# Kernel tuning notes

Measured on AMD Instinct MI355X. Metric: run time of the kernel, lower is better.

Reference implementation:

```python
import jax, jax.numpy as jnp
import numpy as np

BS, D, H = 65536, 768, 12
DK = D // H // 2  # 32
EPS = 1e-6

def setup_inputs() -> dict:
    key = jax.random.key(0)
    ks = jax.random.split(key, 4)
    scale = 1.0 / np.sqrt(D)
    return {
        "x": jax.random.normal(ks[0], (BS, D), dtype=jnp.float32),
        "Wq": jax.random.normal(ks[1], (D, D), dtype=jnp.float32) * scale,
        "Wk": jax.random.normal(ks[2], (D, D), dtype=jnp.float32) * scale,
        "Wv": jax.random.normal(ks[3], (D, D), dtype=jnp.float32) * scale,
        "gamma": jnp.ones((D,), dtype=jnp.float32),
        "beta": jnp.zeros((D,), dtype=jnp.float32),
    }

def reference(x, Wq, Wk, Wv, gamma, beta):
    bs = x.shape[0]
    # LayerNorm (eps=1e-6)
    mu = jnp.mean(x, axis=-1, keepdims=True)
    var = jnp.mean(jnp.square(x - mu), axis=-1, keepdims=True)
    xn = (x - mu) / jnp.sqrt(var + EPS) * gamma + beta
    # QKV projections (nn.Linear, no bias: y = x @ W.T), split feature dim as (h, 2, d_k)
    q = (xn @ Wq.T).reshape(bs, H, 2, DK)
    k = (xn @ Wk.T).reshape(bs, H, 2, DK)
    v = (xn @ Wv.T).reshape(bs, H, 2, DK)
    # tiny 2x2 attention per head
    scores = jnp.einsum('bhpd,bhqd->bhpq', q, k) / np.sqrt(DK)
    attn = jax.nn.softmax(scores, axis=-1)
    out = jnp.einsum('bhpq,bhqd->bhpd', attn, v).reshape(bs, D)
    return out + x
```

## Files before the change

kernel.cpp:

```cpp
#include <hip/hip_runtime.h>

typedef _Float16 f16;
typedef _Float16 f16x8 __attribute__((ext_vector_type(8)));
typedef _Float16 f16x4 __attribute__((ext_vector_type(4)));
typedef float f32x16 __attribute__((ext_vector_type(16)));

#define BS 65536
#define D 768
#define H 12
#define RB 256
#define NBLK ((BS / RB) * H)
#define W_ELEMS ((size_t)D * D)
#define XN_ELEMS ((size_t)BS * D)

typedef const __attribute__((address_space(1))) void gvoid_t;
typedef __attribute__((address_space(3))) void lvoid_t;

__global__ __launch_bounds__(256, 4) void ln_kernel(const float* __restrict__ x,
                                                    const float* __restrict__ gamma,
                                                    const float* __restrict__ beta,
                                                    f16* __restrict__ xn) {
  int wave = threadIdx.x >> 6, lane = threadIdx.x & 63;
  size_t row = (size_t)blockIdx.x * 4 + wave;
  const float4* xr = (const float4*)(x + row * D) + lane * 3;
  float4 v0 = xr[0], v1 = xr[1], v2 = xr[2];
  float sum = (v0.x + v0.y) + (v0.z + v0.w) + (v1.x + v1.y) + (v1.z + v1.w)
            + (v2.x + v2.y) + (v2.z + v2.w);
  float sq = v0.x*v0.x + v0.y*v0.y + v0.z*v0.z + v0.w*v0.w
           + v1.x*v1.x + v1.y*v1.y + v1.z*v1.z + v1.w*v1.w
           + v2.x*v2.x + v2.y*v2.y + v2.z*v2.z + v2.w*v2.w;
#pragma unroll
  for (int d2 = 1; d2 <= 32; d2 <<= 1) {
    sum += __shfl_xor(sum, d2, 64);
    sq  += __shfl_xor(sq,  d2, 64);
  }
  float mu   = sum * (1.0f / D);
  float rstd = rsqrtf(sq * (1.0f / D) - mu * mu + 1e-6f);
  const float4* g4 = (const float4*)(gamma) + lane * 3;
  const float4* b4 = (const float4*)(beta)  + lane * 3;
  float4 g0 = g4[0], g1 = g4[1], g2 = g4[2];
  float4 b0 = b4[0], b1 = b4[1], b2 = b4[2];
  f16* xo = xn + row * D + lane * 12;
  f16x4 o0, o1, o2;
  o0[0] = (f16)((v0.x - mu) * rstd * g0.x + b0.x);
  o0[1] = (f16)((v0.y - mu) * rstd * g0.y + b0.y);
  o0[2] = (f16)((v0.z - mu) * rstd * g0.z + b0.z);
  o0[3] = (f16)((v0.w - mu) * rstd * g0.w + b0.w);
  o1[0] = (f16)((v1.x - mu) * rstd * g1.x + b1.x);
  o1[1] = (f16)((v1.y - mu) * rstd * g1.y + b1.y);
  o1[2] = (f16)((v1.z - mu) * rstd * g1.z + b1.z);
  o1[3] = (f16)((v1.w - mu) * rstd * g1.w + b1.w);
  o2[0] = (f16)((v2.x - mu) * rstd * g2.x + b2.x);
  o2[1] = (f16)((v2.y - mu) * rstd * g2.y + b2.y);
  o2[2] = (f16)((v2.z - mu) * rstd * g2.z + b2.z);
  o2[3] = (f16)((v2.w - mu) * rstd * g2.w + b2.w);
  *(f16x4*)(xo)     = o0;
  *(f16x4*)(xo + 4) = o1;
  *(f16x4*)(xo + 8) = o2;
}

__global__ __launch_bounds__(256, 4) void wconv_kernel(const float* __restrict__ Wq,
                                                       const float* __restrict__ Wk,
                                                       const float* __restrict__ Wv,
                                                       f16* __restrict__ wf) {
  int b = blockIdx.x;
  int m = b / 288;
  size_t e = ((size_t)(b % 288) * 256 + threadIdx.x) * 8;
  const float* src = (m == 0 ? Wq : (m == 1 ? Wk : Wv)) + e;
  float4 v0 = *(const float4*)src;
  float4 v1 = *(const float4*)(src + 4);
  f16x8 o;
  o[0] = (f16)v0.x; o[1] = (f16)v0.y; o[2] = (f16)v0.z; o[3] = (f16)v0.w;
  o[4] = (f16)v1.x; o[5] = (f16)v1.y; o[6] = (f16)v1.z; o[7] = (f16)v1.w;
  *(f16x8*)(wf + (size_t)m * W_ELEMS + e) = o;
}

__global__ __launch_bounds__(256, 2) void qkv_attn_kernel(const f16* __restrict__ xn,
                                                          const f16* __restrict__ wf,
                                                          const float* __restrict__ x,
                                                          float* __restrict__ out) {
  __shared__ f16 sB[2][192 * 64] __attribute__((aligned(16)));

  const int tid  = threadIdx.x;
  const int wave = tid >> 6;
  const int lane = tid & 63;
  const int l31  = lane & 31;
  const int hi   = lane >> 5;

  int bid = blockIdx.x;
  int my  = (bid & 7) * (NBLK / 8) + (bid >> 3);
  int rb  = my / H;
  int h   = my % H;

  unsigned offs[6];
  {
    int rl = wave * 48 + (lane & 7);
    int c  = lane >> 3;
#pragma unroll
    for (int o = 0; o < 6; ++o) {
      int r = rl + o * 8;
      offs[o] = (unsigned)((r >> 6) * (int)W_ELEMS + (h * 64 + (r & 63)) * D + c * 8);
    }
  }

  const int rbase = (l31 >> 3) * 512 + hi * 64 + (l31 & 7) * 8;

  const f16* ap0 = xn + ((size_t)rb * RB + wave * 64 + l31) * D + hi * 8;
  const f16* ap1 = ap0 + (size_t)32 * D;

#define STAGE(KO, BUF)                                                                   \
  {                                                                                      \
    const f16* bp = wf + (KO) * 64;                                                      \
    _Pragma("unroll") for (int o = 0; o < 6; ++o) {                                      \
      __builtin_amdgcn_global_load_lds((gvoid_t*)(bp + offs[o]),                         \
                                       (lvoid_t*)(&sB[BUF][(wave * 6 + o) * 512]),       \
                                       16, 0, 0);                                        \
    }                                                                                    \
  }

  STAGE(0, 0);

  f32x16 acc[6][2];
#pragma unroll
  for (int t = 0; t < 6; ++t)
#pragma unroll
    for (int rt = 0; rt < 2; ++rt)
#pragma unroll
      for (int i = 0; i < 16; ++i) acc[t][rt][i] = 0.f;

  __syncthreads();

#pragma unroll
  for (int ko = 0; ko < 12; ++ko) {
    const int cur = ko & 1;
    if (ko < 11) STAGE(ko + 1, cur ^ 1);
    __builtin_amdgcn_sched_barrier(0);

    const f16* bb = &sB[cur][rbase];
    __builtin_amdgcn_s_setprio(1);
#pragma unroll
    for (int s = 0; s < 4; ++s) {
      f16x8 a0 = *(const f16x8*)(ap0 + ko * 64 + s * 16);
      f16x8 a1 = *(const f16x8*)(ap1 + ko * 64 + s * 16);
#pragma unroll
      for (int t = 0; t < 6; ++t) {
        f16x8 b = *(const f16x8*)(bb + t * 2048 + s * 128);
        acc[t][0] = __builtin_amdgcn_mfma_f32_32x32x16_f16(a0, b, acc[t][0], 0, 0, 0);
        acc[t][1] = __builtin_amdgcn_mfma_f32_32x32x16_f16(a1, b, acc[t][1], 0, 0, 0);
      }
    }
    __builtin_amdgcn_s_setprio(0);
    if (ko < 11) __syncthreads();
  }

  {
    const float scale = 0.17677669529663687f;
#pragma unroll
    for (int rt = 0; rt < 2; ++rt) {
      const size_t grow0 = (size_t)rb * RB + wave * 64 + rt * 32;
#pragma unroll
      for (int g = 0; g < 16; ++g) {
        float q0 = acc[0][rt][g], q1 = acc[1][rt][g];
        float k0 = acc[2][rt][g], k1 = acc[3][rt][g];
        float s00 = q0 * k0, s01 = q0 * k1, s10 = q1 * k0, s11 = q1 * k1;
#pragma unroll
        for (int d2 = 1; d2 <= 16; d2 <<= 1) {
          s00 += __shfl_xor(s00, d2, 64);
          s01 += __shfl_xor(s01, d2, 64);
          s10 += __shfl_xor(s10, d2, 64);
          s11 += __shfl_xor(s11, d2, 64);
        }
        s00 *= scale; s01 *= scale; s10 *= scale; s11 *= scale;
        float mx0 = fmaxf(s00, s01);
        float e00 = __expf(s00 - mx0), e01 = __expf(s01 - mx0);
        float r0 = 1.0f / (e00 + e01);
        float a00 = e00 * r0, a01 = e01 * r0;
        float mx1 = fmaxf(s10, s11);
        float e10 = __expf(s10 - mx1), e11 = __expf(s11 - mx1);
        float r1 = 1.0f / (e10 + e11);
        float a10 = e10 * r1, a11 = e11 * r1;

        int row_w = (g & 3) + 8 * (g >> 2) + 4 * hi;
        const float* xp = x   + (grow0 + row_w) * D + h * 64 + l31;
        float*       op = out + (grow0 + row_w) * D + h * 64 + l31;
        float v0 = acc[4][rt][g], v1 = acc[5][rt][g];
        op[0]  = a00 * v0 + a01 * v1 + xp[0];
        op[32] = a10 * v0 + a11 * v1 + xp[32];
      }
    }
  }
#undef STAGE
}

extern "C" void kernel_launch(void* const* d_in, const int* in_sizes, int n_in,
                              void* d_out, int out_size, void* d_ws, size_t ws_size,
                              hipStream_t stream) {
  const float* x     = (const float*)d_in[0];
  const float* Wq    = (const float*)d_in[1];
  const float* Wk    = (const float*)d_in[2];
  const float* Wv    = (const float*)d_in[3];
  const float* gamma = (const float*)d_in[4];
  const float* beta  = (const float*)d_in[5];
  float* out = (float*)d_out;
  (void)in_sizes; (void)n_in; (void)out_size; (void)ws_size;

  f16* xn = (f16*)d_ws;
  f16* wf = xn + XN_ELEMS;

  ln_kernel<<<dim3(BS / 4), dim3(256), 0, stream>>>(x, gamma, beta, xn);
  wconv_kernel<<<dim3(864), dim3(256), 0, stream>>>(Wq, Wk, Wv, wf);
  qkv_attn_kernel<<<dim3(NBLK), dim3(256), 0, stream>>>(xn, wf, x, out);
}
```

Baseline: 712.6 us.

## Stage A tiles through swizzled LDS, halve row block, coalesce LN stores

The QKV kernel now loads the activation tile into LDS with global_load_lds, double-buffered like the weights. Both A and B tiles get an XOR swizzle, and the row block per workgroup drops from 256 to 128, so each wave does one 32-row MFMA tile. The __syncthreads calls are replaced with explicit vmcnt waits and s_barrier. LayerNorm now handles two rows per wave and stages the fp16 output through LDS for 16-byte coalesced stores. Halving the row block doubles how often the weight slice is refetched per row, and the hand-written waitcnt counts must match the number of issued loads.

Result: no change. 723.4 us (+1.5%).

```diff
diff --git a/kernel.cpp b/kernel.cpp
--- a/kernel.cpp
+++ b/kernel.cpp
@@ -8,7 +8,7 @@
 #define BS 65536
 #define D 768
 #define H 12
-#define RB 256
+#define RB 128
 #define NBLK ((BS / RB) * H)
 #define W_ELEMS ((size_t)D * D)
 #define XN_ELEMS ((size_t)BS * D)
@@ -20,43 +20,62 @@
                                                     const float* __restrict__ gamma,
                                                     const float* __restrict__ beta,
                                                     f16* __restrict__ xn) {
+  __shared__ f16 sRow[4][2 * D];
   int wave = threadIdx.x >> 6, lane = threadIdx.x & 63;
-  size_t row = (size_t)blockIdx.x * 4 + wave;
-  const float4* xr = (const float4*)(x + row * D) + lane * 3;
-  float4 v0 = xr[0], v1 = xr[1], v2 = xr[2];
-  float sum = (v0.x + v0.y) + (v0.z + v0.w) + (v1.x + v1.y) + (v1.z + v1.w)
-            + (v2.x + v2.y) + (v2.z + v2.w);
-  float sq = v0.x*v0.x + v0.y*v0.y + v0.z*v0.z + v0.w*v0.w
-           + v1.x*v1.x + v1.y*v1.y + v1.z*v1.z + v1.w*v1.w
-           + v2.x*v2.x + v2.y*v2.y + v2.z*v2.z + v2.w*v2.w;
+  size_t row0 = ((size_t)blockIdx.x * 4 + wave) * 2;
+  const float4* xr0 = (const float4*)(x + row0 * D) + lane * 3;
+  const float4* xr1 = (const float4*)(x + (row0 + 1) * D) + lane * 3;
+  float4 u0 = xr0[0], u1 = xr0[1], u2 = xr0[2];
+  float4 w0 = xr1[0], w1 = xr1[1], w2 = xr1[2];
+
+  float s0 = (u0.x + u0.y) + (u0.z + u0.w) + (u1.x + u1.y) + (u1.z + u1.w)
+           + (u2.x + u2.y) + (u2.z + u2.w);
+  float q0 = u0.x*u0.x + u0.y*u0.y + u0.z*u0.z + u0.w*u0.w
+           + u1.x*u1.x + u1.y*u1.y + u1.z*u1.z + u1.w*u1.w
+           + u2.x*u2.x + u2.y*u2.y + u2.z*u2.z + u2.w*u2.w;
+  float s1 = (w0.x + w0.y) + (w0.z + w0.w) + (w1.x + w1.y) + (w1.z + w1.w)
+           + (w2.x + w2.y) + (w2.z + w2.w);
+  float q1 = w0.x*w0.x + w0.y*w0.y + w0.z*w0.z + w0.w*w0.w
+           + w1.x*w1.x + w1.y*w1.y + w1.z*w1.z + w1.w*w1.w
+           + w2.x*w2.x + w2.y*w2.y + w2.z*w2.z + w2.w*w2.w;
 #pragma unroll
   for (int d2 = 1; d2 <= 32; d2 <<= 1) {
-    sum += __shfl_xor(sum, d2, 64);
-    sq  += __shfl_xor(sq,  d2, 64);
-  }
-  float mu   = sum * (1.0f / D);
-  float rstd = rsqrtf(sq * (1.0f / D) - mu * mu + 1e-6f);
+    s0 += __shfl_xor(s0, d2, 64); q0 += __shfl_xor(q0, d2, 64);
+    s1 += __shfl_xor(s1, d2, 64); q1 += __shfl_xor(q1, d2, 64);
+  }
+  float mu0 = s0 * (1.0f / D), rs0 = rsqrtf(q0 * (1.0f / D) - mu0 * mu0 + 1e-6f);
+  float mu1 = s1 * (1.0f / D), rs1 = rsqrtf(q1 * (1.0f / D) - mu1 * mu1 + 1e-6f);
+
   const float4* g4 = (const float4*)(gamma) + lane * 3;
   const float4* b4 = (const float4*)(beta)  + lane * 3;
   float4 g0 = g4[0], g1 = g4[1], g2 = g4[2];
   float4 b0 = b4[0], b1 = b4[1], b2 = b4[2];
-  f16* xo = xn + row * D + lane * 12;
-  f16x4 o0, o1, o2;
-  o0[0] = (f16)((v0.x - mu) * rstd * g0.x + b0.x);
-  o0[1] = (f16)((v0.y - mu) * rstd * g0.y + b0.y);
-  o0[2] = (f16)((v0.z - mu) * rstd * g0.z + b0.z);
-  o0[3] = (f16)((v0.w - mu) * rstd * g0.w + b0.w);
-  o1[0] = (f16)((v1.x - mu) * rstd * g1.x + b1.x);
-  o1[1] = (f16)((v1.y - mu) * rstd * g1.y + b1.y);
-  o1[2] = (f16)((v1.z - mu) * rstd * g1.z + b1.z);
-  o1[3] = (f16)((v1.w - mu) * rstd * g1.w + b1.w);
-  o2[0] = (f16)((v2.x - mu) * rstd * g2.x + b2.x);
-  o2[1] = (f16)((v2.y - mu) * rstd * g2.y + b2.y);
-  o2[2] = (f16)((v2.z - mu) * rstd * g2.z + b2.z);
-  o2[3] = (f16)((v2.w - mu) * rstd * g2.w + b2.w);
-  *(f16x4*)(xo)     = o0;
-  *(f16x4*)(xo + 4) = o1;
-  *(f16x4*)(xo + 8) = o2;
+
+  f16* sw = &sRow[wave][lane * 12];
+#define NRM4(dst, off, V, G, B, MU, RS)                        \
+  { f16x4 o;                                                   \
+    o[0] = (f16)((V.x - MU) * RS * G.x + B.x);                 \
+    o[1] = (f16)((V.y - MU) * RS * G.y + B.y);                 \
+    o[2] = (f16)((V.z - MU) * RS * G.z + B.z);                 \
+    o[3] = (f16)((V.w - MU) * RS * G.w + B.w);                 \
+    *(f16x4*)(dst + off) = o; }
+  NRM4(sw, 0, u0, g0, b0, mu0, rs0)
+  NRM4(sw, 4, u1, g1, b1, mu0, rs0)
+  NRM4(sw, 8, u2, g2, b2, mu0, rs0)
+  NRM4(sw, D + 0, w0, g0, b0, mu1, rs1)
+  NRM4(sw, D + 4, w1, g1, b1, mu1, rs1)
+  NRM4(sw, D + 8, w2, g2, b2, mu1, rs1)
+#undef NRM4
+  __builtin_amdgcn_sched_barrier(0);
+  asm volatile("s_waitcnt lgkmcnt(0)" ::: "memory");
+  __builtin_amdgcn_sched_barrier(0);
+  f16* xo = xn + row0 * D;
+#pragma unroll
+  for (int j = 0; j < 3; ++j) {
+    int c = j * 64 + lane;
+    f16x8 v = *(const f16x8*)(&sRow[wave][c * 8]);
+    *(f16x8*)(xo + c * 8) = v;
+  }
 }
 
 __global__ __launch_bounds__(256, 4) void wconv_kernel(const float* __restrict__ Wq,
@@ -79,6 +98,7 @@
                                                           const f16* __restrict__ wf,
                                                           const float* __restrict__ x,
                                                           float* __restrict__ out) {
+  __shared__ f16 sA[2][RB * 64]  __attribute__((aligned(16)));
   __shared__ f16 sB[2][192 * 64] __attribute__((aligned(16)));
 
   const int tid  = threadIdx.x;
@@ -92,101 +112,107 @@
   int rb  = my / H;
   int h   = my % H;
 
-  unsigned offs[6];
-  {
-    int rl = wave * 48 + (lane & 7);
-    int c  = lane >> 3;
-#pragma unroll
-    for (int o = 0; o < 6; ++o) {
-      int r = rl + o * 8;
-      offs[o] = (unsigned)((r >> 6) * (int)W_ELEMS + (h * 64 + (r & 63)) * D + c * 8);
-    }
-  }
-
-  const int rbase = (l31 >> 3) * 512 + hi * 64 + (l31 & 7) * 8;
-
-  const f16* ap0 = xn + ((size_t)rb * RB + wave * 64 + l31) * D + hi * 8;
-  const f16* ap1 = ap0 + (size_t)32 * D;
+  const int ri = lane >> 3;
+  const int ci = lane & 7;
+
+  const f16* abase = xn + (size_t)rb * RB * D;
+  unsigned aoffs[4];
+#pragma unroll
+  for (int o = 0; o < 4; ++o)
+    aoffs[o] = (unsigned)((wave * 32 + o * 8 + ri) * D + ((ci ^ ri) * 8));
+
+  unsigned boffs[6];
+#pragma unroll
+  for (int o = 0; o < 6; ++o) {
+    int n = wave * 48 + o * 8 + ri;
+    boffs[o] = (unsigned)((n >> 6) * (int)W_ELEMS + (h * 64 + (n & 63)) * D + ((ci ^ ri) * 8));
+  }
+
+  const int q7 = l31 & 7;
+  int aoff[4], coff[4];
+#pragma unroll
+  for (int s = 0; s < 4; ++s) {
+    int kc = s * 2 + hi;
+    aoff[s] = (wave * 32 + l31) * 64 + ((kc ^ q7) * 8);
+    coff[s] = l31 * 64 + ((kc ^ q7) * 8);
+  }
 
 #define STAGE(KO, BUF)                                                                   \
   {                                                                                      \
-    const f16* bp = wf + (KO) * 64;                                                      \
-    _Pragma("unroll") for (int o = 0; o < 6; ++o) {                                      \
-      __builtin_amdgcn_global_load_lds((gvoid_t*)(bp + offs[o]),                         \
-                                       (lvoid_t*)(&sB[BUF][(wave * 6 + o) * 512]),       \
+    _Pragma("unroll") for (int o = 0; o < 4; ++o) {                                      \
+      __builtin_amdgcn_global_load_lds((gvoid_t*)(abase + aoffs[o] + (KO) * 64),         \
+                                       (lvoid_t*)(&sA[BUF][(wave * 32 + o * 8) * 64]),   \
                                        16, 0, 0);                                        \
     }                                                                                    \
+    _Pragma("unroll") for (int o = 0; o < 6; ++o) {                                      \
+      __builtin_amdgcn_global_load_lds((gvoid_t*)(wf + boffs[o] + (KO) * 64),            \
+                                       (lvoid_t*)(&sB[BUF][(wave * 48 + o * 8) * 64]),   \
+                                       16, 0, 0);                                        \
+    }                                                                                    \
   }
 
   STAGE(0, 0);
 
-  f32x16 acc[6][2];
+  f32x16 acc[6];
 #pragma unroll
   for (int t = 0; t < 6; ++t)
 #pragma unroll
-    for (int rt = 0; rt < 2; ++rt)
-#pragma unroll
-      for (int i = 0; i < 16; ++i) acc[t][rt][i] = 0.f;
-
-  __syncthreads();
+    for (int i = 0; i < 16; ++i) acc[t][i] = 0.f;
 
 #pragma unroll
   for (int ko = 0; ko < 12; ++ko) {
     const int cur = ko & 1;
     if (ko < 11) STAGE(ko + 1, cur ^ 1);
-    __builtin_amdgcn_sched_barrier(0);
-
-    const f16* bb = &sB[cur][rbase];
+
+    if (ko < 11) asm volatile("s_waitcnt vmcnt(10)\n\ts_barrier" ::: "memory");
+    else         asm volatile("s_waitcnt vmcnt(0)\n\ts_barrier" ::: "memory");
+
     __builtin_amdgcn_s_setprio(1);
 #pragma unroll
     for (int s = 0; s < 4; ++s) {
-      f16x8 a0 = *(const f16x8*)(ap0 + ko * 64 + s * 16);
-      f16x8 a1 = *(const f16x8*)(ap1 + ko * 64 + s * 16);
+      f16x8 a = *(const f16x8*)(&sA[cur][aoff[s]]);
 #pragma unroll
       for (int t = 0; t < 6; ++t) {
-        f16x8 b = *(const f16x8*)(bb + t * 2048 + s * 128);
-        acc[t][0] = __builtin_amdgcn_mfma_f32_32x32x16_f16(a0, b, acc[t][0], 0, 0, 0);
-        acc[t][1] = __builtin_amdgcn_mfma_f32_32x32x16_f16(a1, b, acc[t][1], 0, 0, 0);
+        f16x8 b = *(const f16x8*)(&sB[cur][coff[s] + t * 2048]);
+        acc[t] = __builtin_amdgcn_mfma_f32_32x32x16_f16(a, b, acc[t], 0, 0, 0);
       }
     }
     __builtin_amdgcn_s_setprio(0);
-    if (ko < 11) __syncthreads();
+
+    if (ko < 11) asm volatile("s_barrier" ::: "memory");
   }
 
   {
+    const size_t grow0 = (size_t)rb * RB + wave * 32;
     const float scale = 0.17677669529663687f;
 #pragma unroll
-    for (int rt = 0; rt < 2; ++rt) {
-      const size_t grow0 = (size_t)rb * RB + wave * 64 + rt * 32;
-#pragma unroll
-      for (int g = 0; g < 16; ++g) {
-        float q0 = acc[0][rt][g], q1 = acc[1][rt][g];
-        float k0 = acc[2][rt][g], k1 = acc[3][rt][g];
-        float s00 = q0 * k0, s01 = q0 * k1, s10 = q1 * k0, s11 = q1 * k1;
-#pragma unroll
-        for (int d2 = 1; d2 <= 16; d2 <<= 1) {
-          s00 += __shfl_xor(s00, d2, 64);
-          s01 += __shfl_xor(s01, d2, 64);
-          s10 += __shfl_xor(s10, d2, 64);
-          s11 += __shfl_xor(s11, d2, 64);
-        }
-        s00 *= scale; s01 *= scale; s10 *= scale; s11 *= scale;
-        float mx0 = fmaxf(s00, s01);
-        float e00 = __expf(s00 - mx0), e01 = __expf(s01 - mx0);
-        float r0 = 1.0f / (e00 + e01);
-        float a00 = e00 * r0, a01 = e01 * r0;
-        float mx1 = fmaxf(s10, s11);
-        float e10 = __expf(s10 - mx1), e11 = __expf(s11 - mx1);
-        float r1 = 1.0f / (e10 + e11);
-        float a10 = e10 * r1, a11 = e11 * r1;
-
-        int row_w = (g & 3) + 8 * (g >> 2) + 4 * hi;
-        const float* xp = x   + (grow0 + row_w) * D + h * 64 + l31;
-        float*       op = out + (grow0 + row_w) * D + h * 64 + l31;
-        float v0 = acc[4][rt][g], v1 = acc[5][rt][g];
-        op[0]  = a00 * v0 + a01 * v1 + xp[0];
-        op[32] = a10 * v0 + a11 * v1 + xp[32];
+    for (int g = 0; g < 16; ++g) {
+      float q0 = acc[0][g], q1 = acc[1][g];
+      float k0 = acc[2][g], k1 = acc[3][g];
+      float s00 = q0 * k0, s01 = q0 * k1, s10 = q1 * k0, s11 = q1 * k1;
+#pragma unroll
+      for (int d2 = 1; d2 <= 16; d2 <<= 1) {
+        s00 += __shfl_xor(s00, d2, 64);
+        s01 += __shfl_xor(s01, d2, 64);
+        s10 += __shfl_xor(s10, d2, 64);
+        s11 += __shfl_xor(s11, d2, 64);
       }
+      s00 *= scale; s01 *= scale; s10 *= scale; s11 *= scale;
+      float mx0 = fmaxf(s00, s01);
+      float e00 = __expf(s00 - mx0), e01 = __expf(s01 - mx0);
+      float r0 = 1.0f / (e00 + e01);
+      float a00 = e00 * r0, a01 = e01 * r0;
+      float mx1 = fmaxf(s10, s11);
+      float e10 = __expf(s10 - mx1), e11 = __expf(s11 - mx1);
+      float r1 = 1.0f / (e10 + e11);
+      float a10 = e10 * r1, a11 = e11 * r1;
+
+      int row_w = (g & 3) + 8 * (g >> 2) + 4 * hi;
+      const float* xp = x   + (grow0 + row_w) * D + h * 64 + l31;
+      float*       op = out + (grow0 + row_w) * D + h * 64 + l31;
+      float v0 = acc[4][g], v1 = acc[5][g];
+      op[0]  = a00 * v0 + a01 * v1 + xp[0];
+      op[32] = a10 * v0 + a11 * v1 + xp[32];
     }
   }
 #undef STAGE
@@ -207,7 +233,7 @@
   f16* xn = (f16*)d_ws;
   f16* wf = xn + XN_ELEMS;
 
-  ln_kernel<<<dim3(BS / 4), dim3(256), 0, stream>>>(x, gamma, beta, xn);
+  ln_kernel<<<dim3(BS / 8), dim3(256), 0, stream>>>(x, gamma, beta, xn);
   wconv_kernel<<<dim3(864), dim3(256), 0, stream>>>(Wq, Wk, Wv, wf);
   qkv_attn_kernel<<<dim3(NBLK), dim3(256), 0, stream>>>(xn, wf, x, out);
 }
```
